# Optimization experiments

Measured on AMD Instinct MI355X. Metric: run time of the kernel, lower is better.

The kernel has to match this reference:

```python
import jax, jax.numpy as jnp
import numpy as np

B, D, H = 8192, 256, 512


def setup_inputs() -> dict:
    key = jax.random.key(0)
    ks = jax.random.split(key, 25)
    inp = {
        "x": jax.random.normal(ks[0], (B, D), jnp.float32),
        "h_t": jax.random.normal(ks[1], (B, H), jnp.float32),
        "h_s": jax.random.normal(ks[2], (B, H), jnp.float32),
        "c_t": jax.random.normal(ks[3], (B, H), jnp.float32),
        "c_s": jax.random.normal(ks[4], (B, H), jnp.float32),
    }
    names = ["Ui", "Wti", "Wsi", "bi", "Us", "Wts", "Wss", "bs",
             "Ut", "Wtt", "Wst", "bt", "Uo", "Wto", "Wso", "bo",
             "Uc", "Wtc", "Wsc", "bc"]
    shapes = {"U": (D, H), "W": (H, H), "b": (H,)}
    scale = 0.02  # keep activations in a sane range
    for i, n in enumerate(names):
        s = shapes["U"] if n[0] == "U" else (shapes["b"] if n[0] == "b" else shapes["W"])
        inp[n] = jax.random.normal(ks[5 + i], s, jnp.float32) * scale
    return inp


def reference(x, h_t, h_s, c_t, c_s,
              Ui, Wti, Wsi, bi, Us, Wts, Wss, bs,
              Ut, Wtt, Wst, bt, Uo, Wto, Wso, bo,
              Uc, Wtc, Wsc, bc):
    # Fuse the 15 small GEMMs into 3 concatenated GEMMs: [B,D]@[D,5H] etc.
    U = jnp.concatenate([Ui, Us, Ut, Uo, Uc], axis=1)      # [D, 5H]
    Wt = jnp.concatenate([Wti, Wts, Wtt, Wto, Wtc], axis=1)  # [H, 5H]
    Ws = jnp.concatenate([Wsi, Wss, Wst, Wso, Wsc], axis=1)  # [H, 5H]
    b = jnp.concatenate([bi, bs, bt, bo, bc])                # [5H]
    gates = x @ U + h_t @ Wt + h_s @ Ws + b                  # [B, 5H]
    g_i, g_fs, g_ft, g_o, g_c = jnp.split(gates, 5, axis=1)
    i_n = jax.nn.sigmoid(g_i)
    f_s_n = jax.nn.sigmoid(g_fs)
    f_t_n = jax.nn.sigmoid(g_ft)
    o_n = jax.nn.sigmoid(g_o)
    c_n = jnp.tanh(g_c)
    c_h = i_n * c_n + f_t_n * c_t + f_s_n * c_s
    h = o_n * jnp.tanh(c_h)
    return (h, c_h)
```

## Files before the change

### kernel.cpp

```cpp
#include <hip/hip_runtime.h>
#include <hip/hip_bf16.h>
#include <cstdint>
#include <cstddef>

#define B_  8192
#define D_  256
#define H_  512
#define K_  1280
#define N_  2560
#define NT_ 320

typedef short short8  __attribute__((ext_vector_type(8)));
typedef float f32x4   __attribute__((ext_vector_type(4)));
typedef float f32x16  __attribute__((ext_vector_type(16)));

__device__ __forceinline__ float sigf(float x)     { return 1.f / (1.f + __expf(-x)); }
__device__ __forceinline__ float tanhfast(float x) { return 1.f - 2.f / (__expf(2.f * x) + 1.f); }

struct WPtrs {
    const float* U[5];
    const float* Wt[5];
    const float* Ws[5];
};

__global__ void prep_kernel(const float* __restrict__ x, const float* __restrict__ ht,
                            const float* __restrict__ hs, WPtrs p,
                            __hip_bfloat16* __restrict__ A, __hip_bfloat16* __restrict__ WT) {
    __shared__ __hip_bfloat16 tile[64][72];
    int bid = blockIdx.x;
    if (bid < 5120) {
        int t = bid * 256 + threadIdx.x;
        int idx8 = t * 8;
        int b = idx8 / K_;
        int k = idx8 - b * K_;
        const float* src;
        if (k < D_)            src = x  + (size_t)b * D_ + k;
        else if (k < D_ + H_)  src = ht + (size_t)b * H_ + (k - D_);
        else                   src = hs + (size_t)b * H_ + (k - D_ - H_);
        f32x4 v0 = *(const f32x4*)(src);
        f32x4 v1 = *(const f32x4*)(src + 4);
        union { short8 s; __hip_bfloat16 h[8]; } o;
        o.h[0] = __float2bfloat16(v0[0]); o.h[1] = __float2bfloat16(v0[1]);
        o.h[2] = __float2bfloat16(v0[2]); o.h[3] = __float2bfloat16(v0[3]);
        o.h[4] = __float2bfloat16(v1[0]); o.h[5] = __float2bfloat16(v1[1]);
        o.h[6] = __float2bfloat16(v1[2]); o.h[7] = __float2bfloat16(v1[3]);
        *(short8*)(A + idx8) = o.s;
    } else {
        int bid2 = bid - 5120;
        int hblk = bid2 & 7;
        int kblk = (bid2 >> 3) % 20;
        int g    = bid2 / 160;
        int k0 = kblk * 64;
        int h0 = hblk * 64;
        const float* src; int kl0;
        if (k0 < 256)      { src = p.U[g];  kl0 = k0; }
        else if (k0 < 768) { src = p.Wt[g]; kl0 = k0 - 256; }
        else               { src = p.Ws[g]; kl0 = k0 - 768; }
        int tid = threadIdx.x;
        int tk = tid >> 6;
        int th = tid & 63;
        for (int r = 0; r < 16; ++r) {
            int kl = r * 4 + tk;
            tile[kl][th] = __float2bfloat16(src[(size_t)(kl0 + kl) * H_ + h0 + th]);
        }
        __syncthreads();
        for (int r = 0; r < 16; ++r) {
            int hl = r * 4 + tk;
            int h  = h0 + hl;
            int np = (h >> 5) * 160 + g * 32 + (h & 31);
            WT[(size_t)np * K_ + k0 + th] = tile[th][hl];
        }
    }
}

#define GLD16(gp, lp)                                                              \
    __builtin_amdgcn_global_load_lds(                                              \
        (const __attribute__((address_space(1))) unsigned int*)(gp),               \
        (__attribute__((address_space(3))) unsigned int*)(lp), 16, 0, 0)

__global__ __launch_bounds__(256, 2) void gemm_fused_kernel(
    const __hip_bfloat16* __restrict__ A, const __hip_bfloat16* __restrict__ WT,
    const float* __restrict__ ct, const float* __restrict__ cs,
    const float* __restrict__ bi, const float* __restrict__ bfs,
    const float* __restrict__ bft, const float* __restrict__ bo,
    const float* __restrict__ bc, float* __restrict__ out) {
    __shared__ alignas(16) unsigned short sA[128 * 32];
    __shared__ alignas(16) unsigned short sB[NT_ * 32];

    int tid = threadIdx.x;
    int m0 = blockIdx.x * 128;
    int n0 = blockIdx.y * NT_;
    int wid  = tid >> 6, lane = tid & 63;
    int wm   = wid >> 1;
    int wn   = wid & 1;
    int half = lane >> 5, l31 = lane & 31;

    int hg = blockIdx.y * 2 + wn;
    int h  = hg * 32 + l31;
    float Bi = bi[h], Bfs = bfs[h], Bft = bft[h], Bo = bo[h], Bc = bc[h];

    f32x16 acc[2][5];
#pragma unroll
    for (int i = 0; i < 2; ++i)
#pragma unroll
        for (int j = 0; j < 5; ++j)
            acc[i][j] = (f32x16)(0.f);

    const __hip_bfloat16* aSrc[2]; unsigned short* aDst[2];
#pragma unroll
    for (int i = 0; i < 2; ++i) {
        int c = tid + 256 * i;
        int row = c >> 2, pos = c & 3;
        int kc = pos ^ ((row >> 1) & 3);
        aSrc[i] = A + (size_t)(m0 + row) * K_ + kc * 8;
        aDst[i] = sA + c * 8;
    }
    const __hip_bfloat16* bSrc[5]; unsigned short* bDst[5];
#pragma unroll
    for (int i = 0; i < 5; ++i) {
        int c = tid + 256 * i;
        int row = c >> 2, pos = c & 3;
        int kc = pos ^ ((row >> 1) & 3);
        bSrc[i] = WT + (size_t)(n0 + row) * K_ + kc * 8;
        bDst[i] = sB + c * 8;
    }

    int arow[2], brow[5];
#pragma unroll
    for (int i = 0; i < 2; ++i) arow[i] = wm * 64 + i * 32 + l31;
#pragma unroll
    for (int j = 0; j < 5; ++j) brow[j] = wn * 160 + j * 32 + l31;

    for (int k0 = 0; k0 < K_; k0 += 32) {
#pragma unroll
        for (int i = 0; i < 2; ++i) GLD16(aSrc[i] + k0, aDst[i]);
#pragma unroll
        for (int i = 0; i < 5; ++i) GLD16(bSrc[i] + k0, bDst[i]);
        __syncthreads();

#pragma unroll
        for (int ks = 0; ks < 2; ++ks) {
            short8 a[2], b[5];
#pragma unroll
            for (int i = 0; i < 2; ++i) {
                int pos = (ks * 2 + half) ^ ((arow[i] >> 1) & 3);
                a[i] = *(const short8*)(sA + arow[i] * 32 + pos * 8);
            }
#pragma unroll
            for (int j = 0; j < 5; ++j) {
                int pos = (ks * 2 + half) ^ ((brow[j] >> 1) & 3);
                b[j] = *(const short8*)(sB + brow[j] * 32 + pos * 8);
            }
#pragma unroll
            for (int j = 0; j < 5; ++j)
#pragma unroll
                for (int i = 0; i < 2; ++i)
                    acc[i][j] = __builtin_amdgcn_mfma_f32_32x32x16_bf16(a[i], b[j], acc[i][j], 0, 0, 0);
        }
        __syncthreads();
    }

#pragma unroll
    for (int i = 0; i < 2; ++i) {
        int rbase = m0 + wm * 64 + i * 32 + 4 * half;
#pragma unroll
        for (int r = 0; r < 16; ++r) {
            int row = rbase + (r & 3) + 8 * (r >> 2);
            size_t idx = (size_t)row * H_ + h;
            float i_n  = sigf(acc[i][0][r] + Bi);
            float fs_n = sigf(acc[i][1][r] + Bfs);
            float ft_n = sigf(acc[i][2][r] + Bft);
            float o_n  = sigf(acc[i][3][r] + Bo);
            float c_n  = tanhfast(acc[i][4][r] + Bc);
            float ch   = i_n * c_n + ft_n * ct[idx] + fs_n * cs[idx];
            out[idx] = o_n * tanhfast(ch);
            out[(size_t)B_ * H_ + idx] = ch;
        }
    }
}

struct AllW {
    const float* U[5];
    const float* Wt[5];
    const float* Ws[5];
    const float* bias[5];
};

__global__ __launch_bounds__(512) void fallback_kernel(const float* __restrict__ x,
                                                       const float* __restrict__ ht,
                                                       const float* __restrict__ hs,
                                                       const float* __restrict__ ct,
                                                       const float* __restrict__ cs,
                                                       AllW w, float* __restrict__ out) {
    __shared__ float arow[K_];
    int b = blockIdx.x;
    int h = threadIdx.x;
    for (int k = h; k < K_; k += 512) {
        float v;
        if (k < D_)           v = x[b * D_ + k];
        else if (k < D_ + H_) v = ht[b * H_ + k - D_];
        else                  v = hs[b * H_ + k - D_ - H_];
        arow[k] = v;
    }
    __syncthreads();
    float g[5];
    for (int gi = 0; gi < 5; ++gi) {
        float s = w.bias[gi][h];
        const float* U = w.U[gi];
        for (int k = 0; k < D_; ++k) s += arow[k] * U[(size_t)k * H_ + h];
        const float* Wt = w.Wt[gi];
        for (int k = 0; k < H_; ++k) s += arow[D_ + k] * Wt[(size_t)k * H_ + h];
        const float* Ws = w.Ws[gi];
        for (int k = 0; k < H_; ++k) s += arow[D_ + H_ + k] * Ws[(size_t)k * H_ + h];
        g[gi] = s;
    }
    int idx = b * H_ + h;
    float i_n = sigf(g[0]), fs_n = sigf(g[1]), ft_n = sigf(g[2]), o_n = sigf(g[3]);
    float c_n = tanhfast(g[4]);
    float ch  = i_n * c_n + ft_n * ct[idx] + fs_n * cs[idx];
    out[idx] = o_n * tanhfast(ch);
    out[(size_t)B_ * H_ + idx] = ch;
}

extern "C" void kernel_launch(void* const* d_in, const int* in_sizes, int n_in,
                              void* d_out, int out_size, void* d_ws, size_t ws_size,
                              hipStream_t stream) {
    const float* x  = (const float*)d_in[0];
    const float* ht = (const float*)d_in[1];
    const float* hs = (const float*)d_in[2];
    const float* ct = (const float*)d_in[3];
    const float* cs = (const float*)d_in[4];

    WPtrs wp;
    AllW  aw;
    const float* bias[5];
    for (int g = 0; g < 5; ++g) {
        wp.U[g]  = (const float*)d_in[5 + g * 4 + 0];
        wp.Wt[g] = (const float*)d_in[5 + g * 4 + 1];
        wp.Ws[g] = (const float*)d_in[5 + g * 4 + 2];
        bias[g]  = (const float*)d_in[5 + g * 4 + 3];
        aw.U[g] = wp.U[g]; aw.Wt[g] = wp.Wt[g]; aw.Ws[g] = wp.Ws[g]; aw.bias[g] = bias[g];
    }
    float* out = (float*)d_out;

    size_t szA = (size_t)B_ * K_ * 2;
    size_t szW = (size_t)N_ * K_ * 2;

    if (ws_size >= szA + szW) {
        __hip_bfloat16* Abf = (__hip_bfloat16*)d_ws;
        __hip_bfloat16* WT  = (__hip_bfloat16*)((char*)d_ws + szA);

        prep_kernel<<<5120 + 800, 256, 0, stream>>>(x, ht, hs, wp, Abf, WT);
        gemm_fused_kernel<<<dim3(B_ / 128, N_ / NT_), 256, 0, stream>>>(
            Abf, WT, ct, cs, bias[0], bias[1], bias[2], bias[3], bias[4], out);
    } else {
        fallback_kernel<<<B_, 512, 0, stream>>>(x, ht, hs, ct, cs, aw, out);
    }
}
```

Measured before the change: 235.3 us.

## Double-buffer LDS tiles in fused GEMM to overlap loads with MFMA

Shared-memory A/B tiles are double-buffered: the next K-slice is issued via global_load_lds into the alternate buffer while MFMAs run on the current one, leaving one barrier per iteration instead of two. MFMA sections are wrapped in s_setprio to favor math issue. The prep kernel transpose tile padding is changed from 72 to 66 columns. LDS use per block doubles, which may reduce occupancy at 2 blocks/CU.

```diff
diff --git a/kernel.cpp b/kernel.cpp
--- a/kernel.cpp
+++ b/kernel.cpp
@@ -26,7 +26,7 @@
 __global__ void prep_kernel(const float* __restrict__ x, const float* __restrict__ ht,
                             const float* __restrict__ hs, WPtrs p,
                             __hip_bfloat16* __restrict__ A, __hip_bfloat16* __restrict__ WT) {
-    __shared__ __hip_bfloat16 tile[64][72];
+    __shared__ __hip_bfloat16 tile[64][66];
     int bid = blockIdx.x;
     if (bid < 5120) {
         int t = bid * 256 + threadIdx.x;
@@ -84,8 +84,8 @@
     const float* __restrict__ bi, const float* __restrict__ bfs,
     const float* __restrict__ bft, const float* __restrict__ bo,
     const float* __restrict__ bc, float* __restrict__ out) {
-    __shared__ alignas(16) unsigned short sA[128 * 32];
-    __shared__ alignas(16) unsigned short sB[NT_ * 32];
+    __shared__ alignas(16) unsigned short sA[2][128 * 32];
+    __shared__ alignas(16) unsigned short sB[2][NT_ * 32];
 
     int tid = threadIdx.x;
     int m0 = blockIdx.x * 128;
@@ -106,23 +106,23 @@
         for (int j = 0; j < 5; ++j)
             acc[i][j] = (f32x16)(0.f);
 
-    const __hip_bfloat16* aSrc[2]; unsigned short* aDst[2];
+    const __hip_bfloat16* aSrc[2]; int aOff[2];
 #pragma unroll
     for (int i = 0; i < 2; ++i) {
         int c = tid + 256 * i;
         int row = c >> 2, pos = c & 3;
         int kc = pos ^ ((row >> 1) & 3);
         aSrc[i] = A + (size_t)(m0 + row) * K_ + kc * 8;
-        aDst[i] = sA + c * 8;
-    }
-    const __hip_bfloat16* bSrc[5]; unsigned short* bDst[5];
+        aOff[i] = c * 8;
+    }
+    const __hip_bfloat16* bSrc[5]; int bOff[5];
 #pragma unroll
     for (int i = 0; i < 5; ++i) {
         int c = tid + 256 * i;
         int row = c >> 2, pos = c & 3;
         int kc = pos ^ ((row >> 1) & 3);
         bSrc[i] = WT + (size_t)(n0 + row) * K_ + kc * 8;
-        bDst[i] = sB + c * 8;
+        bOff[i] = c * 8;
     }
 
     int arow[2], brow[5];
@@ -131,12 +131,21 @@
 #pragma unroll
     for (int j = 0; j < 5; ++j) brow[j] = wn * 160 + j * 32 + l31;
 
+#pragma unroll
+    for (int i = 0; i < 2; ++i) GLD16(aSrc[i], &sA[0][aOff[i]]);
+#pragma unroll
+    for (int i = 0; i < 5; ++i) GLD16(bSrc[i], &sB[0][bOff[i]]);
+    __syncthreads();
+
+    int cur = 0;
     for (int k0 = 0; k0 < K_; k0 += 32) {
-#pragma unroll
-        for (int i = 0; i < 2; ++i) GLD16(aSrc[i] + k0, aDst[i]);
-#pragma unroll
-        for (int i = 0; i < 5; ++i) GLD16(bSrc[i] + k0, bDst[i]);
-        __syncthreads();
+        if (k0 + 32 < K_) {
+            int nxt = cur ^ 1;
+#pragma unroll
+            for (int i = 0; i < 2; ++i) GLD16(aSrc[i] + k0 + 32, &sA[nxt][aOff[i]]);
+#pragma unroll
+            for (int i = 0; i < 5; ++i) GLD16(bSrc[i] + k0 + 32, &sB[nxt][bOff[i]]);
+        }
 
 #pragma unroll
         for (int ks = 0; ks < 2; ++ks) {
@@ -144,20 +153,23 @@
 #pragma unroll
             for (int i = 0; i < 2; ++i) {
                 int pos = (ks * 2 + half) ^ ((arow[i] >> 1) & 3);
-                a[i] = *(const short8*)(sA + arow[i] * 32 + pos * 8);
+                a[i] = *(const short8*)(&sA[cur][arow[i] * 32 + pos * 8]);
             }
 #pragma unroll
             for (int j = 0; j < 5; ++j) {
                 int pos = (ks * 2 + half) ^ ((brow[j] >> 1) & 3);
-                b[j] = *(const short8*)(sB + brow[j] * 32 + pos * 8);
+                b[j] = *(const short8*)(&sB[cur][brow[j] * 32 + pos * 8]);
             }
+            __builtin_amdgcn_s_setprio(1);
 #pragma unroll
             for (int j = 0; j < 5; ++j)
 #pragma unroll
                 for (int i = 0; i < 2; ++i)
                     acc[i][j] = __builtin_amdgcn_mfma_f32_32x32x16_bf16(a[i], b[j], acc[i][j], 0, 0, 0);
+            __builtin_amdgcn_s_setprio(0);
         }
         __syncthreads();
+        cur ^= 1;
     }
 
 #pragma unroll
```

Measured after the change: 239.9 us. About the same (+1.9%).
